# Kernel optimization log

Measured on AMD Instinct MI355X. Metric: run time of the kernel, lower is better.

The kernel has to match this reference:

```python
import jax, jax.numpy as jnp
import numpy as np

B, N, DIN, DOUT = 16, 256, 64, 64
TEMP = 2.0          # temperatures[0]
POOL_K = 0.5        # pool_ratios[0]
BN_EPS = 1e-5


def setup_inputs() -> dict:
    key = jax.random.key(0)
    ks = jax.random.split(key, 8)
    g = lambda i, shape: (jax.random.normal(ks[i], shape, jnp.float32) * 0.08)
    return {
        "x": jax.random.normal(ks[0], (B, N, DIN), jnp.float32),
        # GraphAttentionLayer params
        "W_att": g(1, (DIN, DOUT)), "b_att": jnp.zeros((DOUT,), jnp.float32),
        "att_w": g(2, (DOUT,)),                      # att_weight [DOUT,1] squeezed
        "W_pwa": g(3, (DIN, DOUT)), "b_pwa": jnp.zeros((DOUT,), jnp.float32),
        "W_pna": g(4, (DIN, DOUT)), "b_pna": jnp.zeros((DOUT,), jnp.float32),
        "bn_scale": jnp.ones((DOUT,), jnp.float32),
        "bn_bias": jnp.zeros((DOUT,), jnp.float32),
        # GraphPool params
        "pool_w": g(5, (DOUT,)), "pool_b": jnp.zeros((), jnp.float32),
    }


def reference(x, W_att, b_att, att_w, W_pwa, b_pwa, W_pna, b_pna,
              bn_scale, bn_bias, pool_w, pool_b):
    # --- GraphAttentionLayer (eval mode: dropout = identity) ---
    # pairwise node multiplication: [B, i, j, DIN]
    pm = x[:, :, None, :] * x[:, None, :, :]
    att = jnp.tanh(jnp.einsum('bijd,de->bije', pm, W_att) + b_att)   # [B,N,N,DOUT]
    logits = jnp.einsum('bije,e->bij', att, att_w) / TEMP            # [B,N,N]
    # torch softmax over dim=-2 of [B,i,j,1] == axis j (the aggregated axis)
    A = jax.nn.softmax(logits, axis=2)                               # [B,N,N]
    agg = jnp.einsum('bij,bjd->bid', A, x)                           # [B,N,DIN]
    h = (agg @ W_pwa + b_pwa) + (x @ W_pna + b_pna)                  # [B,N,DOUT]
    # BatchNorm1d eval with running_mean=0, running_var=1
    h = h * (bn_scale / jnp.sqrt(1.0 + BN_EPS)) + bn_bias
    h = jax.nn.selu(h)
    # --- GraphPool (eval mode: dropout = identity) ---
    scores = jax.nn.sigmoid(h @ pool_w + pool_b)                     # [B,N]
    k = max(int(N * POOL_K), 1)
    _, idx = jax.lax.top_k(scores, k)                                # [B,k]
    hw = h * scores[:, :, None]
    out = jnp.take_along_axis(hw, idx[:, :, None], axis=1)           # [B,k,DOUT]
    return out
```

## Files before the change

### kernel.cpp

```cpp
#include <hip/hip_runtime.h>
#include <hip/hip_bf16.h>
#include <math.h>

#define BB 16
#define NN 256
#define DD 64
#define KTOP 128

typedef short s16x8 __attribute__((ext_vector_type(8)));
typedef float f32x4 __attribute__((ext_vector_type(4)));

typedef union { s16x8 v; unsigned u[4]; } frag_u;
typedef union { __hip_bfloat162 b2; unsigned u; } cvu;

__device__ __forceinline__ float asf(unsigned u){ union{unsigned u;float f;}c; c.u=u; return c.f; }

__device__ __forceinline__ void split2(float v0, float v1, unsigned& hu, unsigned& lu) {
    cvu c; c.b2 = __float22bfloat162_rn(make_float2(v0, v1));
    unsigned h = c.u;
    float l0 = v0 - asf(h << 16);
    float l1 = v1 - asf(h & 0xffff0000u);
    c.b2 = __float22bfloat162_rn(make_float2(l0, l1));
    hu = h; lu = c.u;
}

__global__ __launch_bounds__(512, 6) void k_fused(
    const float* __restrict__ x, const float* __restrict__ W_att,
    const float* __restrict__ b_att, const float* __restrict__ att_w,
    const float* __restrict__ Wpwa, const float* __restrict__ bpwa,
    const float* __restrict__ Wpna, const float* __restrict__ bpna,
    const float* __restrict__ bnsc, const float* __restrict__ bnbi,
    const float* __restrict__ poolw, const float* __restrict__ poolb,
    float* __restrict__ hbuf, float* __restrict__ scores)
{
    const int ig = blockIdx.x;
    const int b  = blockIdx.y;
    const int tid = threadIdx.x;
    const int w = tid >> 6, lane = tid & 63;
    const int quad = lane >> 4, c16 = lane & 15;
    const int jb = w * 32;
    const int ibase = ig * 4;

    __shared__ s16x8 sB[2][2][4][2][64];
    __shared__ float sXi[4 * 64];
    __shared__ float sL[4][256];
    __shared__ float sAgg[4][64];
    __shared__ float sBatt[64];
    __shared__ float sAww[64];

    if (tid < 256) sXi[tid] = x[(b * NN + ibase + (tid >> 6)) * DD + (tid & 63)];
    if (tid < 64) sBatt[tid] = b_att[tid];
    else if (tid < 128) sAww[tid - 64] = att_w[tid - 64];

    const float L2E2 = 2.8853900817779268f;

    float halfS;
    {
        float sa = 0.0f;
        #pragma unroll
        for (int mt = 0; mt < 4; ++mt) {
            float4 a4 = ((const float4*)att_w)[mt * 4 + quad];
            sa += (a4.x + a4.y) + (a4.z + a4.w);
        }
        sa += __shfl_xor(sa, 16);
        sa += __shfl_xor(sa, 32);
        halfS = 0.5f * sa;
    }

    const int bks = w >> 2, bmt = w & 3;

    frag_u Xh[2][2], Xl[2][2];
    #pragma unroll
    for (int jt = 0; jt < 2; ++jt) {
        #pragma unroll
        for (int ks = 0; ks < 2; ++ks) {
            const float* xr = &x[(b * NN + jb + jt * 16 + c16) * DD + ks * 32 + quad * 8];
            float4 a0 = *(const float4*)xr;
            float4 a1 = *(const float4*)(xr + 4);
            split2(a0.x, a0.y, Xh[jt][ks].u[0], Xl[jt][ks].u[0]);
            split2(a0.z, a0.w, Xh[jt][ks].u[1], Xl[jt][ks].u[1]);
            split2(a1.x, a1.y, Xh[jt][ks].u[2], Xl[jt][ks].u[2]);
            split2(a1.z, a1.w, Xh[jt][ks].u[3], Xl[jt][ks].u[3]);
        }
    }
    __syncthreads();

    {
        const float* xr = &sXi[0 * 64 + bks * 32 + quad * 8];
        float4 c0 = *(const float4*)xr;
        float4 c1 = *(const float4*)(xr + 4);
        float xiv[8] = {c0.x,c0.y,c0.z,c0.w,c1.x,c1.y,c1.z,c1.w};
        const float* wp = &W_att[(bks * 32 + quad * 8) * 64 + bmt * 16 + c16];
        frag_u bh, bl;
        split2(wp[0] * xiv[0], wp[64] * xiv[1], bh.u[0], bl.u[0]);
        split2(wp[128] * xiv[2], wp[192] * xiv[3], bh.u[1], bl.u[1]);
        split2(wp[256] * xiv[4], wp[320] * xiv[5], bh.u[2], bl.u[2]);
        split2(wp[384] * xiv[6], wp[448] * xiv[7], bh.u[3], bl.u[3]);
        sB[0][bks][bmt][0][lane] = bh.v;
        sB[0][bks][bmt][1][lane] = bl.v;
    }

    #pragma unroll
    for (int ii = 0; ii < 4; ++ii) {
        __syncthreads();

        if (ii < 3) {
            const float* xr = &sXi[(ii + 1) * 64 + bks * 32 + quad * 8];
            float4 c0 = *(const float4*)xr;
            float4 c1 = *(const float4*)(xr + 4);
            float xiv[8] = {c0.x,c0.y,c0.z,c0.w,c1.x,c1.y,c1.z,c1.w};
            const float* wp = &W_att[(bks * 32 + quad * 8) * 64 + bmt * 16 + c16];
            frag_u bh, bl;
            split2(wp[0] * xiv[0], wp[64] * xiv[1], bh.u[0], bl.u[0]);
            split2(wp[128] * xiv[2], wp[192] * xiv[3], bh.u[1], bl.u[1]);
            split2(wp[256] * xiv[4], wp[320] * xiv[5], bh.u[2], bl.u[2]);
            split2(wp[384] * xiv[6], wp[448] * xiv[7], bh.u[3], bl.u[3]);
            sB[(ii + 1) & 1][bks][bmt][0][lane] = bh.v;
            sB[(ii + 1) & 1][bks][bmt][1][lane] = bl.v;
        }

        const int cur = ii & 1;
        float s0 = 0.0f, s1 = 0.0f;

        #pragma unroll
        for (int eth = 0; eth < 2; ++eth) {
            f32x4 acc[2][2];
            #pragma unroll
            for (int e2 = 0; e2 < 2; ++e2) {
                f32x4 bi = *(const f32x4*)&sBatt[(eth * 2 + e2) * 16 + quad * 4];
                acc[e2][0] = bi;
                acc[e2][1] = bi;
            }

            #pragma unroll
            for (int ks = 0; ks < 2; ++ks) {
                #pragma unroll
                for (int e2 = 0; e2 < 2; ++e2) {
                    const int mt = eth * 2 + e2;
                    s16x8 ah = sB[cur][ks][mt][0][lane];
                    s16x8 al = sB[cur][ks][mt][1][lane];
                    #pragma unroll
                    for (int jt = 0; jt < 2; ++jt) {
                        acc[e2][jt] = __builtin_amdgcn_mfma_f32_16x16x32_bf16(ah, Xh[jt][ks].v, acc[e2][jt], 0, 0, 0);
                        acc[e2][jt] = __builtin_amdgcn_mfma_f32_16x16x32_bf16(al, Xh[jt][ks].v, acc[e2][jt], 0, 0, 0);
                        acc[e2][jt] = __builtin_amdgcn_mfma_f32_16x16x32_bf16(ah, Xl[jt][ks].v, acc[e2][jt], 0, 0, 0);
                    }
                }
            }

            #pragma unroll
            for (int e2 = 0; e2 < 2; ++e2) {
                const int mt = eth * 2 + e2;
                f32x4 awwv = *(const f32x4*)&sAww[mt * 16 + quad * 4];
                #pragma unroll
                for (int r = 0; r < 4; ++r) {
                    {
                        float arg = acc[e2][0][r] * L2E2;
                        float m = __builtin_amdgcn_exp2f(arg);
                        float rc = __builtin_amdgcn_rcpf(m + 1.0f);
                        s0 = fmaf(awwv[r], rc, s0);
                    }
                    {
                        float arg = acc[e2][1][r] * L2E2;
                        float m = __builtin_amdgcn_exp2f(arg);
                        float rc = __builtin_amdgcn_rcpf(m + 1.0f);
                        s1 = fmaf(awwv[r], rc, s1);
                    }
                }
            }
        }

        s0 += __shfl_xor(s0, 16);
        s0 += __shfl_xor(s0, 32);
        s1 += __shfl_xor(s1, 16);
        s1 += __shfl_xor(s1, 32);
        if (quad == 0) {
            sL[ii][jb + c16]      = halfS - s0;
            sL[ii][jb + 16 + c16] = halfS - s1;
        }
    }
    __syncthreads();

    if (w < 4) {
        const int i = ibase + w;
        float* row = sL[w];
        float lg0 = row[lane], lg1 = row[lane + 64], lg2 = row[lane + 128], lg3 = row[lane + 192];
        float m = fmaxf(fmaxf(lg0, lg1), fmaxf(lg2, lg3));
        #pragma unroll
        for (int off = 32; off; off >>= 1) m = fmaxf(m, __shfl_xor(m, off));
        float e0 = __expf(lg0 - m), e1 = __expf(lg1 - m), e2 = __expf(lg2 - m), e3 = __expf(lg3 - m);
        float ssum = e0 + e1 + e2 + e3;
        #pragma unroll
        for (int off = 32; off; off >>= 1) ssum += __shfl_xor(ssum, off);
        float inv = 1.0f / ssum;
        row[lane] = e0 * inv; row[lane + 64] = e1 * inv;
        row[lane + 128] = e2 * inv; row[lane + 192] = e3 * inv;
        __asm__ volatile("s_waitcnt lgkmcnt(0)" ::: "memory");

        float ag0 = 0.f, ag1 = 0.f, ag2 = 0.f, ag3 = 0.f;
        const float4* A4 = (const float4*)row;
        const float* xb = &x[(b * NN) * DD];
        #pragma unroll 8
        for (int jq = 0; jq < 64; ++jq) {
            float4 a = A4[jq];
            int j = jq * 4;
            ag0 = fmaf(a.x, xb[(j + 0) * DD + lane], ag0);
            ag1 = fmaf(a.y, xb[(j + 1) * DD + lane], ag1);
            ag2 = fmaf(a.z, xb[(j + 2) * DD + lane], ag2);
            ag3 = fmaf(a.w, xb[(j + 3) * DD + lane], ag3);
        }
        sAgg[w][lane] = (ag0 + ag1) + (ag2 + ag3);
        __asm__ volatile("s_waitcnt lgkmcnt(0)" ::: "memory");

        double hacc = (double)bpwa[lane] + (double)bpna[lane];
        #pragma unroll 4
        for (int d = 0; d < 64; ++d) {
            hacc += (double)sAgg[w][d] * (double)Wpwa[d * DD + lane]
                  + (double)sXi[w * 64 + d] * (double)Wpna[d * DD + lane];
        }
        const double bnmul = 0.99999500003749968750e0;
        double hb = hacc * ((double)bnsc[lane] * bnmul) + (double)bnbi[lane];
        float hf = (float)hb;
        const float LAM = 1.0507009873554805f, ALP = 1.6732632423543772f;
        float hs = hf > 0.0f ? LAM * hf : LAM * ALP * (__expf(hf) - 1.0f);
        hbuf[((b * NN) + i) * DD + lane] = hs;

        double z = (double)hs * (double)poolw[lane];
        #pragma unroll
        for (int off = 32; off; off >>= 1) z += __shfl_xor(z, off);
        if (lane == 0) {
            double zz = z + (double)poolb[0];
            scores[b * NN + i] = (float)(1.0 / (1.0 + exp(-zz)));
        }
    }
}

__global__ __launch_bounds__(256) void k_topk(
    const float* __restrict__ scores, const float* __restrict__ hbuf,
    float* __restrict__ out)
{
    const int c = blockIdx.x;
    const int b = blockIdx.y;
    const int t = threadIdx.x;
    __shared__ float ss[256];
    __shared__ int   perm[16];
    ss[t] = scores[b * NN + t];
    __syncthreads();
    const float my = ss[t];
    int rank = 0;
    #pragma unroll 8
    for (int j = 0; j < 256; ++j) {
        float v = ss[j];
        rank += (v > my) || (v == my && j < t);
    }
    if ((rank >> 4) == c) perm[rank & 15] = t;
    __syncthreads();
    #pragma unroll
    for (int m = t; m < 16 * DD; m += 256) {
        int r = m >> 6, e = m & 63;
        int i = perm[r];
        out[(b * KTOP + c * 16 + r) * DD + e] = hbuf[((b * NN) + i) * DD + e] * ss[i];
    }
}

extern "C" void kernel_launch(void* const* d_in, const int* in_sizes, int n_in,
                              void* d_out, int out_size, void* d_ws, size_t ws_size,
                              hipStream_t stream) {
    const float* x        = (const float*)d_in[0];
    const float* W_att    = (const float*)d_in[1];
    const float* b_att    = (const float*)d_in[2];
    const float* att_w    = (const float*)d_in[3];
    const float* W_pwa    = (const float*)d_in[4];
    const float* b_pwa    = (const float*)d_in[5];
    const float* W_pna    = (const float*)d_in[6];
    const float* b_pna    = (const float*)d_in[7];
    const float* bn_scale = (const float*)d_in[8];
    const float* bn_bias  = (const float*)d_in[9];
    const float* pool_w   = (const float*)d_in[10];
    const float* pool_b   = (const float*)d_in[11];

    float* hbuf    = (float*)d_ws;
    float* scoresW = hbuf + BB * NN * DD;
    float* out     = (float*)d_out;

    k_fused<<<dim3(64, BB), 512, 0, stream>>>(x, W_att, b_att, att_w,
                                              W_pwa, b_pwa, W_pna, b_pna,
                                              bn_scale, bn_bias, pool_w, pool_b,
                                              hbuf, scoresW);
    k_topk<<<dim3(8, BB), 256, 0, stream>>>(scoresW, hbuf, out);
}
```

Before: 139.6 us.

## Exploit pairwise logit symmetry to compute only upper-triangular blocks

Since the pairwise product x_i*x_j is symmetric, logits[i,j]=logits[j,i]. Each logits block now skips column groups below its row range and writes both its rows and the mirrored columns into a global NxN logit buffer. Softmax, aggregation, projection, SELU and pooling scores move into a new second kernel that reads this buffer. This roughly halves the MFMA and tanh work, at the cost of an extra launch, a global round-trip of the full logit matrix with strided transposed stores, and load imbalance across blocks.

```diff
diff --git a/kernel.cpp b/kernel.cpp
--- a/kernel.cpp
+++ b/kernel.cpp
@@ -24,27 +24,24 @@
     hu = h; lu = c.u;
 }
 
-__global__ __launch_bounds__(512, 6) void k_fused(
+__global__ __launch_bounds__(512, 6) void k_logits(
     const float* __restrict__ x, const float* __restrict__ W_att,
     const float* __restrict__ b_att, const float* __restrict__ att_w,
-    const float* __restrict__ Wpwa, const float* __restrict__ bpwa,
-    const float* __restrict__ Wpna, const float* __restrict__ bpna,
-    const float* __restrict__ bnsc, const float* __restrict__ bnbi,
-    const float* __restrict__ poolw, const float* __restrict__ poolb,
-    float* __restrict__ hbuf, float* __restrict__ scores)
+    float* __restrict__ U)
 {
     const int ig = blockIdx.x;
     const int b  = blockIdx.y;
     const int tid = threadIdx.x;
     const int w = tid >> 6, lane = tid & 63;
     const int quad = lane >> 4, c16 = lane & 15;
-    const int jb = w * 32;
     const int ibase = ig * 4;
+    const int G = ig >> 3;
+    const bool active = w < (8 - G);
+    const int jb = (G + w) * 32;
 
     __shared__ s16x8 sB[2][2][4][2][64];
     __shared__ float sXi[4 * 64];
     __shared__ float sL[4][256];
-    __shared__ float sAgg[4][64];
     __shared__ float sBatt[64];
     __shared__ float sAww[64];
 
@@ -70,17 +67,19 @@
     const int bks = w >> 2, bmt = w & 3;
 
     frag_u Xh[2][2], Xl[2][2];
-    #pragma unroll
-    for (int jt = 0; jt < 2; ++jt) {
+    if (active) {
         #pragma unroll
-        for (int ks = 0; ks < 2; ++ks) {
-            const float* xr = &x[(b * NN + jb + jt * 16 + c16) * DD + ks * 32 + quad * 8];
-            float4 a0 = *(const float4*)xr;
-            float4 a1 = *(const float4*)(xr + 4);
-            split2(a0.x, a0.y, Xh[jt][ks].u[0], Xl[jt][ks].u[0]);
-            split2(a0.z, a0.w, Xh[jt][ks].u[1], Xl[jt][ks].u[1]);
-            split2(a1.x, a1.y, Xh[jt][ks].u[2], Xl[jt][ks].u[2]);
-            split2(a1.z, a1.w, Xh[jt][ks].u[3], Xl[jt][ks].u[3]);
+        for (int jt = 0; jt < 2; ++jt) {
+            #pragma unroll
+            for (int ks = 0; ks < 2; ++ks) {
+                const float* xr = &x[(b * NN + jb + jt * 16 + c16) * DD + ks * 32 + quad * 8];
+                float4 a0 = *(const float4*)xr;
+                float4 a1 = *(const float4*)(xr + 4);
+                split2(a0.x, a0.y, Xh[jt][ks].u[0], Xl[jt][ks].u[0]);
+                split2(a0.z, a0.w, Xh[jt][ks].u[1], Xl[jt][ks].u[1]);
+                split2(a1.x, a1.y, Xh[jt][ks].u[2], Xl[jt][ks].u[2]);
+                split2(a1.z, a1.w, Xh[jt][ks].u[3], Xl[jt][ks].u[3]);
+            }
         }
     }
     __syncthreads();
@@ -119,119 +118,142 @@
             sB[(ii + 1) & 1][bks][bmt][1][lane] = bl.v;
         }
 
-        const int cur = ii & 1;
-        float s0 = 0.0f, s1 = 0.0f;
-
-        #pragma unroll
-        for (int eth = 0; eth < 2; ++eth) {
-            f32x4 acc[2][2];
+        if (active) {
+            const int cur = ii & 1;
+            float s0 = 0.0f, s1 = 0.0f;
             #pragma unroll
-            for (int e2 = 0; e2 < 2; ++e2) {
-                f32x4 bi = *(const f32x4*)&sBatt[(eth * 2 + e2) * 16 + quad * 4];
-                acc[e2][0] = bi;
-                acc[e2][1] = bi;
-            }
-
-            #pragma unroll
-            for (int ks = 0; ks < 2; ++ks) {
+            for (int eth = 0; eth < 2; ++eth) {
+                f32x4 acc[2][2];
+                #pragma unroll
+                for (int e2 = 0; e2 < 2; ++e2) {
+                    f32x4 bi = *(const f32x4*)&sBatt[(eth * 2 + e2) * 16 + quad * 4];
+                    acc[e2][0] = bi;
+                    acc[e2][1] = bi;
+                }
+                #pragma unroll
+                for (int ks = 0; ks < 2; ++ks) {
+                    #pragma unroll
+                    for (int e2 = 0; e2 < 2; ++e2) {
+                        const int mt = eth * 2 + e2;
+                        s16x8 ah = sB[cur][ks][mt][0][lane];
+                        s16x8 al = sB[cur][ks][mt][1][lane];
+                        #pragma unroll
+                        for (int jt = 0; jt < 2; ++jt) {
+                            acc[e2][jt] = __builtin_amdgcn_mfma_f32_16x16x32_bf16(ah, Xh[jt][ks].v, acc[e2][jt], 0, 0, 0);
+                            acc[e2][jt] = __builtin_amdgcn_mfma_f32_16x16x32_bf16(al, Xh[jt][ks].v, acc[e2][jt], 0, 0, 0);
+                            acc[e2][jt] = __builtin_amdgcn_mfma_f32_16x16x32_bf16(ah, Xl[jt][ks].v, acc[e2][jt], 0, 0, 0);
+                        }
+                    }
+                }
                 #pragma unroll
                 for (int e2 = 0; e2 < 2; ++e2) {
                     const int mt = eth * 2 + e2;
-                    s16x8 ah = sB[cur][ks][mt][0][lane];
-                    s16x8 al = sB[cur][ks][mt][1][lane];
+                    f32x4 awwv = *(const f32x4*)&sAww[mt * 16 + quad * 4];
                     #pragma unroll
-                    for (int jt = 0; jt < 2; ++jt) {
-                        acc[e2][jt] = __builtin_amdgcn_mfma_f32_16x16x32_bf16(ah, Xh[jt][ks].v, acc[e2][jt], 0, 0, 0);
-                        acc[e2][jt] = __builtin_amdgcn_mfma_f32_16x16x32_bf16(al, Xh[jt][ks].v, acc[e2][jt], 0, 0, 0);
-                        acc[e2][jt] = __builtin_amdgcn_mfma_f32_16x16x32_bf16(ah, Xl[jt][ks].v, acc[e2][jt], 0, 0, 0);
+                    for (int r = 0; r < 4; ++r) {
+                        {
+                            float m = __builtin_amdgcn_exp2f(acc[e2][0][r] * L2E2);
+                            s0 = fmaf(awwv[r], __builtin_amdgcn_rcpf(m + 1.0f), s0);
+                        }
+                        {
+                            float m = __builtin_amdgcn_exp2f(acc[e2][1][r] * L2E2);
+                            s1 = fmaf(awwv[r], __builtin_amdgcn_rcpf(m + 1.0f), s1);
+                        }
                     }
                 }
             }
-
-            #pragma unroll
-            for (int e2 = 0; e2 < 2; ++e2) {
-                const int mt = eth * 2 + e2;
-                f32x4 awwv = *(const f32x4*)&sAww[mt * 16 + quad * 4];
-                #pragma unroll
-                for (int r = 0; r < 4; ++r) {
-                    {
-                        float arg = acc[e2][0][r] * L2E2;
-                        float m = __builtin_amdgcn_exp2f(arg);
-                        float rc = __builtin_amdgcn_rcpf(m + 1.0f);
-                        s0 = fmaf(awwv[r], rc, s0);
-                    }
-                    {
-                        float arg = acc[e2][1][r] * L2E2;
-                        float m = __builtin_amdgcn_exp2f(arg);
-                        float rc = __builtin_amdgcn_rcpf(m + 1.0f);
-                        s1 = fmaf(awwv[r], rc, s1);
-                    }
-                }
+            s0 += __shfl_xor(s0, 16);
+            s0 += __shfl_xor(s0, 32);
+            s1 += __shfl_xor(s1, 16);
+            s1 += __shfl_xor(s1, 32);
+            if (quad == 0) {
+                sL[ii][jb + c16]      = halfS - s0;
+                sL[ii][jb + 16 + c16] = halfS - s1;
             }
         }
-
-        s0 += __shfl_xor(s0, 16);
-        s0 += __shfl_xor(s0, 32);
-        s1 += __shfl_xor(s1, 16);
-        s1 += __shfl_xor(s1, 32);
-        if (quad == 0) {
-            sL[ii][jb + c16]      = halfS - s0;
-            sL[ii][jb + 16 + c16] = halfS - s1;
-        }
     }
     __syncthreads();
 
-    if (w < 4) {
-        const int i = ibase + w;
-        float* row = sL[w];
-        float lg0 = row[lane], lg1 = row[lane + 64], lg2 = row[lane + 128], lg3 = row[lane + 192];
-        float m = fmaxf(fmaxf(lg0, lg1), fmaxf(lg2, lg3));
-        #pragma unroll
-        for (int off = 32; off; off >>= 1) m = fmaxf(m, __shfl_xor(m, off));
-        float e0 = __expf(lg0 - m), e1 = __expf(lg1 - m), e2 = __expf(lg2 - m), e3 = __expf(lg3 - m);
-        float ssum = e0 + e1 + e2 + e3;
-        #pragma unroll
-        for (int off = 32; off; off >>= 1) ssum += __shfl_xor(ssum, off);
-        float inv = 1.0f / ssum;
-        row[lane] = e0 * inv; row[lane + 64] = e1 * inv;
-        row[lane + 128] = e2 * inv; row[lane + 192] = e3 * inv;
-        __asm__ volatile("s_waitcnt lgkmcnt(0)" ::: "memory");
-
-        float ag0 = 0.f, ag1 = 0.f, ag2 = 0.f, ag3 = 0.f;
-        const float4* A4 = (const float4*)row;
-        const float* xb = &x[(b * NN) * DD];
-        #pragma unroll 8
-        for (int jq = 0; jq < 64; ++jq) {
-            float4 a = A4[jq];
-            int j = jq * 4;
-            ag0 = fmaf(a.x, xb[(j + 0) * DD + lane], ag0);
-            ag1 = fmaf(a.y, xb[(j + 1) * DD + lane], ag1);
-            ag2 = fmaf(a.z, xb[(j + 2) * DD + lane], ag2);
-            ag3 = fmaf(a.w, xb[(j + 3) * DD + lane], ag3);
-        }
-        sAgg[w][lane] = (ag0 + ag1) + (ag2 + ag3);
-        __asm__ volatile("s_waitcnt lgkmcnt(0)" ::: "memory");
-
-        double hacc = (double)bpwa[lane] + (double)bpna[lane];
-        #pragma unroll 4
-        for (int d = 0; d < 64; ++d) {
-            hacc += (double)sAgg[w][d] * (double)Wpwa[d * DD + lane]
-                  + (double)sXi[w * 64 + d] * (double)Wpna[d * DD + lane];
-        }
-        const double bnmul = 0.99999500003749968750e0;
-        double hb = hacc * ((double)bnsc[lane] * bnmul) + (double)bnbi[lane];
-        float hf = (float)hb;
-        const float LAM = 1.0507009873554805f, ALP = 1.6732632423543772f;
-        float hs = hf > 0.0f ? LAM * hf : LAM * ALP * (__expf(hf) - 1.0f);
-        hbuf[((b * NN) + i) * DD + lane] = hs;
-
-        double z = (double)hs * (double)poolw[lane];
-        #pragma unroll
-        for (int off = 32; off; off >>= 1) z += __shfl_xor(z, off);
-        if (lane == 0) {
-            double zz = z + (double)poolb[0];
-            scores[b * NN + i] = (float)(1.0 / (1.0 + exp(-zz)));
-        }
+    #pragma unroll
+    for (int c = 0; c < 4; ++c) {
+        float* Ur = &U[(b * NN + ibase + c) * NN];
+        for (int j = ibase + tid; j < NN; j += 512) Ur[j] = sL[c][j];
+    }
+    {
+        const int cnt = (NN - (ibase + 4)) * 4;
+        for (int m = tid; m < cnt; m += 512) {
+            int rr = ibase + 4 + (m >> 2);
+            U[(b * NN + rr) * NN + ibase + (m & 3)] = sL[m & 3][rr];
+        }
+    }
+}
+
+__global__ __launch_bounds__(256) void k_soft(
+    const float* __restrict__ x, const float* __restrict__ U,
+    const float* __restrict__ Wpwa, const float* __restrict__ bpwa,
+    const float* __restrict__ Wpna, const float* __restrict__ bpna,
+    const float* __restrict__ bnsc, const float* __restrict__ bnbi,
+    const float* __restrict__ poolw, const float* __restrict__ poolb,
+    float* __restrict__ hbuf, float* __restrict__ scores)
+{
+    const int rg = blockIdx.x;
+    const int b  = blockIdx.y;
+    const int w = threadIdx.x >> 6, lane = threadIdx.x & 63;
+    const int r = rg * 4 + w;
+
+    __shared__ float sA[4][256];
+    __shared__ float sAgg[4][64];
+    __shared__ float sXi[4][64];
+
+    const float* row = &U[(b * NN + r) * NN];
+    float lg0 = row[lane], lg1 = row[lane + 64], lg2 = row[lane + 128], lg3 = row[lane + 192];
+    float m = fmaxf(fmaxf(lg0, lg1), fmaxf(lg2, lg3));
+    #pragma unroll
+    for (int off = 32; off; off >>= 1) m = fmaxf(m, __shfl_xor(m, off));
+    float e0 = __expf(lg0 - m), e1 = __expf(lg1 - m), e2 = __expf(lg2 - m), e3 = __expf(lg3 - m);
+    float ssum = e0 + e1 + e2 + e3;
+    #pragma unroll
+    for (int off = 32; off; off >>= 1) ssum += __shfl_xor(ssum, off);
+    float inv = 1.0f / ssum;
+    sA[w][lane] = e0 * inv; sA[w][lane + 64] = e1 * inv;
+    sA[w][lane + 128] = e2 * inv; sA[w][lane + 192] = e3 * inv;
+    sXi[w][lane] = x[(b * NN + r) * DD + lane];
+    __asm__ volatile("s_waitcnt lgkmcnt(0)" ::: "memory");
+
+    float ag0 = 0.f, ag1 = 0.f, ag2 = 0.f, ag3 = 0.f;
+    const float4* A4 = (const float4*)&sA[w][0];
+    const float* xb = &x[(b * NN) * DD];
+    #pragma unroll 8
+    for (int jq = 0; jq < 64; ++jq) {
+        float4 a = A4[jq];
+        int j = jq * 4;
+        ag0 = fmaf(a.x, xb[(j + 0) * DD + lane], ag0);
+        ag1 = fmaf(a.y, xb[(j + 1) * DD + lane], ag1);
+        ag2 = fmaf(a.z, xb[(j + 2) * DD + lane], ag2);
+        ag3 = fmaf(a.w, xb[(j + 3) * DD + lane], ag3);
+    }
+    sAgg[w][lane] = (ag0 + ag1) + (ag2 + ag3);
+    __asm__ volatile("s_waitcnt lgkmcnt(0)" ::: "memory");
+
+    double hacc = (double)bpwa[lane] + (double)bpna[lane];
+    #pragma unroll 4
+    for (int d = 0; d < 64; ++d) {
+        hacc += (double)sAgg[w][d] * (double)Wpwa[d * DD + lane]
+              + (double)sXi[w][d]  * (double)Wpna[d * DD + lane];
+    }
+    const double bnmul = 0.99999500003749968750e0;
+    double hb = hacc * ((double)bnsc[lane] * bnmul) + (double)bnbi[lane];
+    float hf = (float)hb;
+    const float LAM = 1.0507009873554805f, ALP = 1.6732632423543772f;
+    float hs = hf > 0.0f ? LAM * hf : LAM * ALP * (__expf(hf) - 1.0f);
+    hbuf[(b * NN + r) * DD + lane] = hs;
+
+    double z = (double)hs * (double)poolw[lane];
+    #pragma unroll
+    for (int off = 32; off; off >>= 1) z += __shfl_xor(z, off);
+    if (lane == 0) {
+        double zz = z + (double)poolb[0];
+        scores[b * NN + r] = (float)(1.0 / (1.0 + exp(-zz)));
     }
 }
 
@@ -259,7 +281,7 @@
     for (int m = t; m < 16 * DD; m += 256) {
         int r = m >> 6, e = m & 63;
         int i = perm[r];
-        out[(b * KTOP + c * 16 + r) * DD + e] = hbuf[((b * NN) + i) * DD + e] * ss[i];
+        out[(b * KTOP + c * 16 + r) * DD + e] = hbuf[(b * NN + i) * DD + e] * ss[i];
     }
 }
 
@@ -279,13 +301,14 @@
     const float* pool_w   = (const float*)d_in[10];
     const float* pool_b   = (const float*)d_in[11];
 
-    float* hbuf    = (float*)d_ws;
+    float* U       = (float*)d_ws;
+    float* hbuf    = U + BB * NN * NN;
     float* scoresW = hbuf + BB * NN * DD;
     float* out     = (float*)d_out;
 
-    k_fused<<<dim3(64, BB), 512, 0, stream>>>(x, W_att, b_att, att_w,
-                                              W_pwa, b_pwa, W_pna, b_pna,
-                                              bn_scale, bn_bias, pool_w, pool_b,
-                                              hbuf, scoresW);
+    k_logits<<<dim3(64, BB), 512, 0, stream>>>(x, W_att, b_att, att_w, U);
+    k_soft<<<dim3(64, BB), 256, 0, stream>>>(x, U, W_pwa, b_pwa, W_pna, b_pna,
+                                             bn_scale, bn_bias, pool_w, pool_b,
+                                             hbuf, scoresW);
     k_topk<<<dim3(8, BB), 256, 0, stream>>>(scoresW, hbuf, out);
 }
```

After: 148.6 us. 1.06x slower.

## Process eight query rows per block and use all warps in epilogue

Applied to the files above, without the earlier changes.

Each block now handles 8 rows i instead of 4, which halves the grid to 32x16 blocks and lets every one of the 8 warps run the softmax/aggregation/projection epilogue rather than only half of them. The per-block setup (X fragment build, W_att staging) is amortised over twice as many rows. The FP64 projection loop is split into four independent accumulators to shorten its dependency chain. The trade-off is fewer blocks (512 total) on a many-CU GPU, a no-longer-unrolled ii loop, and more shared memory per block.

```diff
diff --git a/kernel.cpp b/kernel.cpp
--- a/kernel.cpp
+++ b/kernel.cpp
@@ -39,16 +39,16 @@
     const int w = tid >> 6, lane = tid & 63;
     const int quad = lane >> 4, c16 = lane & 15;
     const int jb = w * 32;
-    const int ibase = ig * 4;
+    const int ibase = ig * 8;
 
     __shared__ s16x8 sB[2][2][4][2][64];
-    __shared__ float sXi[4 * 64];
-    __shared__ float sL[4][256];
-    __shared__ float sAgg[4][64];
+    __shared__ float sXi[8 * 64];
+    __shared__ float sL[8][256];
+    __shared__ float sAgg[8][64];
     __shared__ float sBatt[64];
     __shared__ float sAww[64];
 
-    if (tid < 256) sXi[tid] = x[(b * NN + ibase + (tid >> 6)) * DD + (tid & 63)];
+    sXi[tid] = x[(b * NN + ibase + (tid >> 6)) * DD + (tid & 63)];
     if (tid < 64) sBatt[tid] = b_att[tid];
     else if (tid < 128) sAww[tid - 64] = att_w[tid - 64];
 
@@ -100,11 +100,10 @@
         sB[0][bks][bmt][1][lane] = bl.v;
     }
 
-    #pragma unroll
-    for (int ii = 0; ii < 4; ++ii) {
+    for (int ii = 0; ii < 8; ++ii) {
         __syncthreads();
 
-        if (ii < 3) {
+        if (ii < 7) {
             const float* xr = &sXi[(ii + 1) * 64 + bks * 32 + quad * 8];
             float4 c0 = *(const float4*)xr;
             float4 c1 = *(const float4*)(xr + 4);
@@ -131,7 +130,6 @@
                 acc[e2][0] = bi;
                 acc[e2][1] = bi;
             }
-
             #pragma unroll
             for (int ks = 0; ks < 2; ++ks) {
                 #pragma unroll
@@ -147,7 +145,6 @@
                     }
                 }
             }
-
             #pragma unroll
             for (int e2 = 0; e2 < 2; ++e2) {
                 const int mt = eth * 2 + e2;
@@ -155,16 +152,12 @@
                 #pragma unroll
                 for (int r = 0; r < 4; ++r) {
                     {
-                        float arg = acc[e2][0][r] * L2E2;
-                        float m = __builtin_amdgcn_exp2f(arg);
-                        float rc = __builtin_amdgcn_rcpf(m + 1.0f);
-                        s0 = fmaf(awwv[r], rc, s0);
+                        float m = __builtin_amdgcn_exp2f(acc[e2][0][r] * L2E2);
+                        s0 = fmaf(awwv[r], __builtin_amdgcn_rcpf(m + 1.0f), s0);
                     }
                     {
-                        float arg = acc[e2][1][r] * L2E2;
-                        float m = __builtin_amdgcn_exp2f(arg);
-                        float rc = __builtin_amdgcn_rcpf(m + 1.0f);
-                        s1 = fmaf(awwv[r], rc, s1);
+                        float m = __builtin_amdgcn_exp2f(acc[e2][1][r] * L2E2);
+                        s1 = fmaf(awwv[r], __builtin_amdgcn_rcpf(m + 1.0f), s1);
                     }
                 }
             }
@@ -181,7 +174,7 @@
     }
     __syncthreads();
 
-    if (w < 4) {
+    {
         const int i = ibase + w;
         float* row = sL[w];
         float lg0 = row[lane], lg1 = row[lane + 64], lg2 = row[lane + 128], lg3 = row[lane + 192];
@@ -189,7 +182,7 @@
         #pragma unroll
         for (int off = 32; off; off >>= 1) m = fmaxf(m, __shfl_xor(m, off));
         float e0 = __expf(lg0 - m), e1 = __expf(lg1 - m), e2 = __expf(lg2 - m), e3 = __expf(lg3 - m);
-        float ssum = e0 + e1 + e2 + e3;
+        float ssum = (e0 + e1) + (e2 + e3);
         #pragma unroll
         for (int off = 32; off; off >>= 1) ssum += __shfl_xor(ssum, off);
         float inv = 1.0f / ssum;
@@ -212,18 +205,25 @@
         sAgg[w][lane] = (ag0 + ag1) + (ag2 + ag3);
         __asm__ volatile("s_waitcnt lgkmcnt(0)" ::: "memory");
 
-        double hacc = (double)bpwa[lane] + (double)bpna[lane];
+        double h0 = 0.0, h1 = 0.0, h2 = 0.0, h3 = 0.0;
         #pragma unroll 4
-        for (int d = 0; d < 64; ++d) {
-            hacc += (double)sAgg[w][d] * (double)Wpwa[d * DD + lane]
-                  + (double)sXi[w * 64 + d] * (double)Wpna[d * DD + lane];
-        }
+        for (int d = 0; d < 64; d += 4) {
+            h0 += (double)sAgg[w][d + 0] * (double)Wpwa[(d + 0) * DD + lane]
+                + (double)sXi[w * 64 + d + 0] * (double)Wpna[(d + 0) * DD + lane];
+            h1 += (double)sAgg[w][d + 1] * (double)Wpwa[(d + 1) * DD + lane]
+                + (double)sXi[w * 64 + d + 1] * (double)Wpna[(d + 1) * DD + lane];
+            h2 += (double)sAgg[w][d + 2] * (double)Wpwa[(d + 2) * DD + lane]
+                + (double)sXi[w * 64 + d + 2] * (double)Wpna[(d + 2) * DD + lane];
+            h3 += (double)sAgg[w][d + 3] * (double)Wpwa[(d + 3) * DD + lane]
+                + (double)sXi[w * 64 + d + 3] * (double)Wpna[(d + 3) * DD + lane];
+        }
+        double hacc = ((double)bpwa[lane] + (double)bpna[lane]) + ((h0 + h1) + (h2 + h3));
         const double bnmul = 0.99999500003749968750e0;
         double hb = hacc * ((double)bnsc[lane] * bnmul) + (double)bnbi[lane];
         float hf = (float)hb;
         const float LAM = 1.0507009873554805f, ALP = 1.6732632423543772f;
         float hs = hf > 0.0f ? LAM * hf : LAM * ALP * (__expf(hf) - 1.0f);
-        hbuf[((b * NN) + i) * DD + lane] = hs;
+        hbuf[(b * NN + i) * DD + lane] = hs;
 
         double z = (double)hs * (double)poolw[lane];
         #pragma unroll
@@ -259,7 +259,7 @@
     for (int m = t; m < 16 * DD; m += 256) {
         int r = m >> 6, e = m & 63;
         int i = perm[r];
-        out[(b * KTOP + c * 16 + r) * DD + e] = hbuf[((b * NN) + i) * DD + e] * ss[i];
+        out[(b * KTOP + c * 16 + r) * DD + e] = hbuf[(b * NN + i) * DD + e] * ss[i];
     }
 }
 
@@ -283,7 +283,7 @@
     float* scoresW = hbuf + BB * NN * DD;
     float* out     = (float*)d_out;
 
-    k_fused<<<dim3(64, BB), 512, 0, stream>>>(x, W_att, b_att, att_w,
+    k_fused<<<dim3(32, BB), 512, 0, stream>>>(x, W_att, b_att, att_w,
                                               W_pwa, b_pwa, W_pna, b_pna,
                                               bn_scale, bn_bias, pool_w, pool_b,
                                               hbuf, scoresW);
```

New measurement: 141.7 us. About the same (+1.5%).
